# Kernel tuning notes

Measured on AMD Instinct MI355X. Metric: run time of the kernel, lower is better.

The kernel has to match this reference:

```python
import jax, jax.numpy as jnp
import numpy as np

E = 512        # embed_dim
H = 16         # num_heads
R = 8          # num_relation_heads
NH = H - R     # num_normal_heads
HD = E // H    # head_dim
SCALING = HD ** -0.5
B, LQ, LK = 2, 2048, 2048


def setup_inputs() -> dict:
    key = jax.random.key(0)
    ks = jax.random.split(key, 14)
    s = 1.0 / np.sqrt(E)  # keep pre-softmax logits moderate so exp() is stable
    inp = {
        "query": jax.random.normal(ks[0], (B, LQ, E), jnp.float32),
        "key": jax.random.normal(ks[1], (B, LK, E), jnp.float32),
        "value": jax.random.normal(ks[2], (B, LK, E), jnp.float32),
        "relation_weights": jax.random.uniform(ks[3], (B, R, LQ, LK), jnp.float32),
        "Wq": jax.random.normal(ks[4], (E, E), jnp.float32) * s,
        "bq": jnp.zeros((E,), jnp.float32),
        "Wk": jax.random.normal(ks[5], (E, E), jnp.float32) * s,
        "bk": jnp.zeros((E,), jnp.float32),
        "Wv": jax.random.normal(ks[6], (E, E), jnp.float32) * s,
        "bv": jnp.zeros((E,), jnp.float32),
        "Wo": jax.random.normal(ks[7], (E, E), jnp.float32) * s,
        "bo": jnp.zeros((E,), jnp.float32),
        "ln_gamma": jnp.ones((E,), jnp.float32),
        "ln_beta": jnp.zeros((E,), jnp.float32),
    }
    return inp


def reference(query, key, value, relation_weights, Wq, bq, Wk, bk, Wv, bv, Wo, bo, ln_gamma, ln_beta):
    b, lq, _ = query.shape
    lk = key.shape[1]
    # projections; weights stored as [in, out] so y = x @ W + b
    q = (query @ Wq + bq).reshape(b, lq, H, HD)
    k = (key @ Wk + bk).reshape(b, lk, H, HD)
    v = (value @ Wv + bv).reshape(b, lk, H, HD)
    # scores: [B, H, Lq, Lk]
    scores = jnp.einsum("bqhd,bkhd->bhqk", q, k) * SCALING
    # normal heads: standard softmax
    normal_attn = jax.nn.softmax(scores[:, :NH], axis=-1)
    # relation heads: exp(scores) * relation_weights, renormalized
    rel = jnp.exp(scores[:, NH:]) * relation_weights
    rel = rel / (rel.sum(axis=-1, keepdims=True) + 1e-6)
    attn = jnp.concatenate([normal_attn, rel], axis=1)  # [B, H, Lq, Lk]
    # weighted values -> [B, Lq, E]
    out = jnp.einsum("bhqk,bkhd->bqhd", attn, v).reshape(b, lq, E)
    out = out @ Wo + bo
    # LayerNorm (eps=1e-5, torch default)
    mu = out.mean(axis=-1, keepdims=True)
    var = out.var(axis=-1, keepdims=True)
    out = (out - mu) * jax.lax.rsqrt(var + 1e-5) * ln_gamma + ln_beta
    return out
```

## Files before the change

kernel.cpp:

```cpp
#include <hip/hip_runtime.h>


using u16 = unsigned short;
using u32 = unsigned int;

typedef __attribute__((ext_vector_type(8))) short bf16x8;
typedef __attribute__((ext_vector_type(4))) float f32x4;

#define H_  16
#define NH_ 8
#define HD_ 32
#define L_  2048
#define E_  512
#define B_  2
#define M_  4096
#define KSPLIT 2
static constexpr float SCALE_ = 0.1767766952966369f;

__device__ inline u16 f2bf(float x) {
  union { float f; u32 u; } v; v.f = x;
  u32 r = v.u + 0x7FFFu + ((v.u >> 16) & 1u);
  return (u16)(r >> 16);
}
__device__ inline float bf2f(u16 x) {
  union { u32 u; float f; } v; v.u = ((u32)x) << 16; return v.f;
}
__device__ inline u16 f2h(float x) {
  union { _Float16 h; u16 u; } v; v.h = (_Float16)x; return v.u;
}
__device__ inline float h2f(u16 x) {
  union { u16 u; _Float16 h; } v; v.u = x; return (float)v.h;
}

__global__ __launch_bounds__(256) void k_cvt3(const float* __restrict__ a, const float* __restrict__ b,
                                              const float* __restrict__ c,
                                              u16* __restrict__ oa, u16* __restrict__ ob, u16* __restrict__ oc) {
  int w = blockIdx.y;
  const float* s = (w == 0) ? a : (w == 1) ? b : c;
  u16* d = (w == 0) ? oa : (w == 1) ? ob : oc;
  size_t i = ((size_t)blockIdx.x * 256 + threadIdx.x) * 4;
  float4 v = *(const float4*)(s + i);
  uint2 pk;
  pk.x = (u32)f2bf(v.x) | ((u32)f2bf(v.y) << 16);
  pk.y = (u32)f2bf(v.z) | ((u32)f2bf(v.w) << 16);
  *(uint2*)(d + i) = pk;
}

__global__ __launch_bounds__(256) void k_wtrans(const float* __restrict__ Wq, const float* __restrict__ Wk,
                                                const float* __restrict__ Wv, const float* __restrict__ Wo,
                                                u16* __restrict__ Tq, u16* __restrict__ Tk,
                                                u16* __restrict__ Tv, u16* __restrict__ To) {
  int z = blockIdx.z;
  const float* W = (z == 0) ? Wq : (z == 1) ? Wk : (z == 2) ? Wv : Wo;
  u16* T = (z == 0) ? Tq : (z == 1) ? Tk : (z == 2) ? Tv : To;
  __shared__ u16 tile[64][65];
  int r0 = blockIdx.y * 64, c0 = blockIdx.x * 64;
  int tw = threadIdx.x >> 6, tl = threadIdx.x & 63;
#pragma unroll
  for (int i = 0; i < 16; ++i) {
    int r = i * 4 + tw;
    tile[r][tl] = f2bf(W[(size_t)(r0 + r) * E_ + c0 + tl]);
  }
  __syncthreads();
#pragma unroll
  for (int i = 0; i < 16; ++i) {
    int r = i * 4 + tw;
    T[(size_t)(c0 + r) * E_ + r0 + tl] = tile[tl][r];
  }
}

template <int MODE>
__device__ inline void gemm_body(const u16* __restrict__ A, const u16* __restrict__ Bt,
                                 const float* __restrict__ bias, void* __restrict__ out) {
  __shared__ __align__(16) u16 smem[2 * 128 * 72];
  u16* As = smem;
  u16* Bs = smem + 128 * 72;
  const int tid = threadIdx.x;
  const int lane = tid & 63, wid = tid >> 6;
  const int m0 = blockIdx.x * 128, n0 = blockIdx.y * 128;
  const int wm = (wid >> 1) * 64, wn = (wid & 1) * 64;
  const int mrow = lane & 15, quad = lane >> 4;
  f32x4 acc[4][4] = {};
  for (int k0 = 0; k0 < 512; k0 += 64) {
    __syncthreads();
#pragma unroll
    for (int i = 0; i < 4; ++i) {
      int task = i * 256 + tid;
      int r = task >> 3, c = task & 7;
      *(uint4*)(As + r * 72 + c * 8) = *(const uint4*)(A + (size_t)(m0 + r) * 512 + k0 + c * 8);
      *(uint4*)(Bs + r * 72 + c * 8) = *(const uint4*)(Bt + (size_t)(n0 + r) * 512 + k0 + c * 8);
    }
    __syncthreads();
#pragma unroll
    for (int kk = 0; kk < 64; kk += 32) {
      bf16x8 af[4], bfr[4];
#pragma unroll
      for (int f = 0; f < 4; ++f)
        af[f] = *(const bf16x8*)(As + (wm + f * 16 + mrow) * 72 + kk + quad * 8);
#pragma unroll
      for (int f = 0; f < 4; ++f)
        bfr[f] = *(const bf16x8*)(Bs + (wn + f * 16 + mrow) * 72 + kk + quad * 8);
#pragma unroll
      for (int fm = 0; fm < 4; ++fm)
#pragma unroll
        for (int fn = 0; fn < 4; ++fn)
          acc[fm][fn] = __builtin_amdgcn_mfma_f32_16x16x32_bf16(af[fm], bfr[fn], acc[fm][fn], 0, 0, 0);
    }
  }
  if (MODE == 0) {
    __syncthreads();
    u16* wscr = smem + wid * (64 * 72);
#pragma unroll
    for (int fn = 0; fn < 4; ++fn) {
      float bv = bias[n0 + wn + fn * 16 + mrow];
#pragma unroll
      for (int fm = 0; fm < 4; ++fm)
#pragma unroll
        for (int r = 0; r < 4; ++r)
          wscr[(fm * 16 + quad * 4 + r) * 72 + fn * 16 + mrow] = f2bf(acc[fm][fn][r] + bv);
    }
    asm volatile("s_waitcnt lgkmcnt(0)" ::: "memory");
    const int hg0 = (n0 + wn) >> 5;
#pragma unroll
    for (int c = 0; c < 8; ++c) {
      int linear = c * 64 + lane;
      int hh = linear >> 8;
      int rem = linear & 255;
      int lm = rem >> 2, j = rem & 3;
      uint4 vv = *(const uint4*)(wscr + lm * 72 + hh * 32 + j * 8);
      int gm = m0 + wm + lm;
      int bb = gm >> 11, q = gm & (L_ - 1);
      *(uint4*)((u16*)out + (((size_t)(bb * H_ + hg0 + hh)) * L_ + q) * HD_ + j * 8) = vv;
    }
  } else {
#pragma unroll
    for (int fn = 0; fn < 4; ++fn) {
      int gn = n0 + wn + fn * 16 + mrow;
      float bv = bias[gn];
#pragma unroll
      for (int fm = 0; fm < 4; ++fm)
#pragma unroll
        for (int r = 0; r < 4; ++r) {
          int gm = m0 + wm + fm * 16 + quad * 4 + r;
          ((float*)out)[(size_t)gm * E_ + gn] = acc[fm][fn][r] + bv;
        }
    }
  }
}

__global__ __launch_bounds__(256) void k_gemm_qkv(const u16* Xq, const u16* Xk, const u16* Xv,
                                                  const u16* Tq, const u16* Tk, const u16* Tv,
                                                  const float* bq, const float* bk, const float* bv,
                                                  u16* Qb, u16* Kb, u16* Vb) {
  int z = blockIdx.z;
  const u16* A = (z == 0) ? Xq : (z == 1) ? Xk : Xv;
  const u16* T = (z == 0) ? Tq : (z == 1) ? Tk : Tv;
  const float* bi = (z == 0) ? bq : (z == 1) ? bk : bv;
  u16* o = (z == 0) ? Qb : (z == 1) ? Kb : Vb;
  gemm_body<0>(A, T, bi, o);
}

__global__ __launch_bounds__(256) void k_gemm_o(const u16* A, const u16* T, const float* bi, float* Y) {
  gemm_body<1>(A, T, bi, Y);
}

__global__ __launch_bounds__(256) void k_attn(const u16* __restrict__ Qb, const u16* __restrict__ Kb,
                                              const u16* __restrict__ Vb, const float* __restrict__ relw,
                                              u16* __restrict__ Pnum, float* __restrict__ Pden) {
  const int tid = threadIdx.x, lane = tid & 63, wid = tid >> 6;
  const int q0 = blockIdx.x * 64;
  const int h = blockIdx.y;
  const int b = blockIdx.z & (B_ - 1), s = blockIdx.z >> 1;
  const int kbase = s * (L_ / KSPLIT);
  const bool isrel = (h >= NH_);
  const size_t headOff = ((size_t)(b * H_ + h)) * L_ * HD_;
  const float* wbase = isrel ? relw + ((size_t)(b * (H_ - NH_) + (h - NH_))) * L_ * L_ : nullptr;

  __shared__ __align__(16) u16 Qs[64 * 40];
  __shared__ __align__(16) u16 Ks[64 * 40];
  __shared__ __align__(16) u16 Vts[32 * 72];
  __shared__ __align__(16) u16 Ps[4][16 * 72];
  __shared__ __align__(16) u16 Ws[64 * 68];

  {
    int r = tid >> 2, c = tid & 3;
    *(uint4*)(Qs + r * 40 + c * 8) = *(const uint4*)(Qb + headOff + (size_t)(q0 + r) * HD_ + c * 8);
  }
  __syncthreads();
  const int mrow = lane & 15, quad = lane >> 4;
  bf16x8 qa = *(const bf16x8*)(Qs + (wid * 16 + mrow) * 40 + quad * 8);
  f32x4 accd[2] = {};
  float den[4] = {0.f, 0.f, 0.f, 0.f};

  for (int kt = kbase; kt < kbase + L_ / KSPLIT; kt += 64) {
    __syncthreads();
    if (tid < 128) {
      int p = tid >> 2, c = tid & 3;
      const u16* vsrc = Vb + headOff + (size_t)(kt + 2 * p) * HD_ + c * 8;
      uint4 v0 = *(const uint4*)(vsrc);
      uint4 v1 = *(const uint4*)(vsrc + HD_);
      const u16* s0 = (const u16*)&v0;
      const u16* s1 = (const u16*)&v1;
#pragma unroll
      for (int i = 0; i < 8; ++i) {
        u32 pk = (u32)s0[i] | ((u32)s1[i] << 16);
        *(u32*)(Vts + (c * 8 + i) * 72 + 2 * p) = pk;
      }
    } else {
      int t2 = tid - 128;
#pragma unroll
      for (int i = 0; i < 2; ++i) {
        int task = t2 * 2 + i;
        int r = task >> 2, c = task & 3;
        *(uint4*)(Ks + r * 40 + c * 8) = *(const uint4*)(Kb + headOff + (size_t)(kt + r) * HD_ + c * 8);
      }
    }
    if (isrel) {
      int q = tid >> 2, kc = (tid & 3) * 4;
      const float* wsrc = wbase + (size_t)(q0 + q) * L_ + kt + kc;
#pragma unroll
      for (int j = 0; j < 4; ++j) {
        float4 w4 = *(const float4*)(wsrc + j * 16);
        uint2 pk;
        pk.x = (u32)f2bf(w4.x) | ((u32)f2bf(w4.y) << 16);
        pk.y = (u32)f2bf(w4.z) | ((u32)f2bf(w4.w) << 16);
        *(uint2*)(Ws + q * 68 + kc + j * 16) = pk;
      }
    }
    __syncthreads();

    u16* pw = Ps[wid];
#pragma unroll
    for (int f = 0; f < 4; ++f) {
      bf16x8 kb = *(const bf16x8*)(Ks + (f * 16 + mrow) * 40 + quad * 8);
      f32x4 z = {0.f, 0.f, 0.f, 0.f};
      f32x4 sc = __builtin_amdgcn_mfma_f32_16x16x32_bf16(qa, kb, z, 0, 0, 0);
#pragma unroll
      for (int r = 0; r < 4; ++r) {
        float e = __expf(sc[r] * SCALE_);
        if (isrel)
          e *= bf2f(Ws[(wid * 16 + quad * 4 + r) * 68 + f * 16 + mrow]);
        den[r] += e;
        pw[(quad * 4 + r) * 72 + f * 16 + mrow] = f2bf(e);
      }
    }
    asm volatile("s_waitcnt lgkmcnt(0)" ::: "memory");
#pragma unroll
    for (int kk = 0; kk < 2; ++kk) {
      bf16x8 pa = *(const bf16x8*)(pw + mrow * 72 + kk * 32 + quad * 8);
#pragma unroll
      for (int dh = 0; dh < 2; ++dh) {
        bf16x8 vbf = *(const bf16x8*)(Vts + (dh * 16 + mrow) * 72 + kk * 32 + quad * 8);
        accd[dh] = __builtin_amdgcn_mfma_f32_16x16x32_bf16(pa, vbf, accd[dh], 0, 0, 0);
      }
    }
  }

#pragma unroll
  for (int off = 1; off < 16; off <<= 1)
#pragma unroll
    for (int r = 0; r < 4; ++r) den[r] += __shfl_xor(den[r], off, 64);

  const size_t pidx = ((size_t)(s * B_ + b) * H_ + h) * L_;
#pragma unroll
  for (int dh = 0; dh < 2; ++dh)
#pragma unroll
    for (int r = 0; r < 4; ++r) {
      int qg = q0 + wid * 16 + quad * 4 + r;
      Pnum[(pidx + qg) * HD_ + dh * 16 + mrow] = f2h(accd[dh][r]);
    }
  if (mrow == 0) {
    int qg = q0 + wid * 16 + quad * 4;
    float4 dv = {den[0], den[1], den[2], den[3]};
    *(float4*)(Pden + pidx + qg) = dv;
  }
}

__global__ __launch_bounds__(256) void k_combine(const u16* __restrict__ Pnum, const float* __restrict__ Pden,
                                                 u16* __restrict__ AO) {
  int row = blockIdx.x;
  int tid = threadIdx.x;
  int b = row >> 11, q = row & (L_ - 1);
  int e0 = tid * 2;
  int h = e0 >> 5, d = e0 & (HD_ - 1);
  size_t i0 = ((size_t)(0 * B_ + b) * H_ + h) * L_ + q;
  size_t i1 = ((size_t)(1 * B_ + b) * H_ + h) * L_ + q;
  u32 n0 = *(const u32*)(Pnum + i0 * HD_ + d);
  u32 n1 = *(const u32*)(Pnum + i1 * HD_ + d);
  float den = Pden[i0] + Pden[i1] + ((h >= NH_) ? 1e-6f : 0.f);
  float rinv = 1.0f / den;
  float x = (h2f((u16)n0) + h2f((u16)n1)) * rinv;
  float y = (h2f((u16)(n0 >> 16)) + h2f((u16)(n1 >> 16))) * rinv;
  u32 pk = (u32)f2bf(x) | ((u32)f2bf(y) << 16);
  *(u32*)(AO + (size_t)row * E_ + e0) = pk;
}

__global__ __launch_bounds__(256) void k_ln(const float* __restrict__ Y, const float* __restrict__ gamma,
                                            const float* __restrict__ beta, float* __restrict__ out) {
  int row = blockIdx.x, tid = threadIdx.x;
  const float* y = Y + (size_t)row * E_;
  float2 v = *(const float2*)(y + tid * 2);
  float s = v.x + v.y, sq = v.x * v.x + v.y * v.y;
#pragma unroll
  for (int off = 1; off < 64; off <<= 1) {
    s += __shfl_xor(s, off, 64);
    sq += __shfl_xor(sq, off, 64);
  }
  __shared__ float ss[4], ssq[4];
  int wid = tid >> 6, lane = tid & 63;
  if (lane == 0) { ss[wid] = s; ssq[wid] = sq; }
  __syncthreads();
  s = ss[0] + ss[1] + ss[2] + ss[3];
  sq = ssq[0] + ssq[1] + ssq[2] + ssq[3];
  float mean = s * (1.f / E_);
  float var = sq * (1.f / E_) - mean * mean;
  float rstd = rsqrtf(var + 1e-5f);
  float2 g = *(const float2*)(gamma + tid * 2);
  float2 be = *(const float2*)(beta + tid * 2);
  float2 o;
  o.x = (v.x - mean) * rstd * g.x + be.x;
  o.y = (v.y - mean) * rstd * g.y + be.y;
  *(float2*)(out + (size_t)row * E_ + tid * 2) = o;
}

extern "C" void kernel_launch(void* const* d_in, const int* in_sizes, int n_in,
                              void* d_out, int out_size, void* d_ws, size_t ws_size,
                              hipStream_t stream) {
  const float* query = (const float*)d_in[0];
  const float* key   = (const float*)d_in[1];
  const float* value = (const float*)d_in[2];
  const float* relw  = (const float*)d_in[3];
  const float* Wq = (const float*)d_in[4];
  const float* bq = (const float*)d_in[5];
  const float* Wk = (const float*)d_in[6];
  const float* bk = (const float*)d_in[7];
  const float* Wv = (const float*)d_in[8];
  const float* bv = (const float*)d_in[9];
  const float* Wo = (const float*)d_in[10];
  const float* bo = (const float*)d_in[11];
  const float* gamma = (const float*)d_in[12];
  const float* beta  = (const float*)d_in[13];

  char* ws = (char*)d_ws;
  u16* Xq = (u16*)(ws + 0);
  u16* Xk = (u16*)(ws + 4194304);
  u16* Xv = (u16*)(ws + 8388608);
  u16* Tq = (u16*)(ws + 12582912);
  u16* Tk = (u16*)(ws + 13107200);
  u16* Tv = (u16*)(ws + 13631488);
  u16* To = (u16*)(ws + 14155776);
  u16* Qb = (u16*)(ws + 14680064);
  u16* Kb = (u16*)(ws + 18874368);
  u16* Vb = (u16*)(ws + 23068672);
  u16* AO = (u16*)(ws + 27262976);
  u16*   Pnum = (u16*)(ws + 0);
  float* Pden = (float*)(ws + 8388608);
  float* Y = (float*)(ws + 0);

  k_cvt3<<<dim3(2048, 3, 1), 256, 0, stream>>>(query, key, value, Xq, Xk, Xv);
  k_wtrans<<<dim3(8, 8, 4), 256, 0, stream>>>(Wq, Wk, Wv, Wo, Tq, Tk, Tv, To);
  k_gemm_qkv<<<dim3(32, 4, 3), 256, 0, stream>>>(Xq, Xk, Xv, Tq, Tk, Tv, bq, bk, bv, Qb, Kb, Vb);
  k_attn<<<dim3(32, 16, B_ * KSPLIT), 256, 0, stream>>>(Qb, Kb, Vb, relw, Pnum, Pden);
  k_combine<<<M_, 256, 0, stream>>>(Pnum, Pden, AO);
  k_gemm_o<<<dim3(32, 4, 1), 256, 0, stream>>>(AO, To, bo, Y);
  k_ln<<<M_, 256, 0, stream>>>(Y, gamma, beta, (float*)d_out);
}
```

Measured before the change: 494.0 us.

## Prefetch next K/V/relation tiles into registers and shrink attention LDS footprint

The attention kernel now issues global loads for the next key tile's K, V and relation weights into registers right after the barrier, so they overlap with the current tile's MFMA and exp work. It also aliases the Q staging buffer with the relation-weight buffer, tightens LDS row strides, and sets a launch-bounds occupancy hint of 6 so more blocks can share a CU. The cost is extra live registers (two uint4 plus four float4) and possible LDS bank conflicts from the new padding strides.

```diff
diff --git a/kernel.cpp b/kernel.cpp
--- a/kernel.cpp
+++ b/kernel.cpp
@@ -164,75 +164,96 @@
   gemm_body<1>(A, T, bi, Y);
 }
 
-__global__ __launch_bounds__(256) void k_attn(const u16* __restrict__ Qb, const u16* __restrict__ Kb,
-                                              const u16* __restrict__ Vb, const float* __restrict__ relw,
-                                              u16* __restrict__ Pnum, float* __restrict__ Pden) {
+__global__ __launch_bounds__(256, 6) void k_attn(const u16* __restrict__ Qb, const u16* __restrict__ Kb,
+                                                 const u16* __restrict__ Vb, const float* __restrict__ relw,
+                                                 u16* __restrict__ Pnum, float* __restrict__ Pden) {
   const int tid = threadIdx.x, lane = tid & 63, wid = tid >> 6;
   const int q0 = blockIdx.x * 64;
   const int h = blockIdx.y;
   const int b = blockIdx.z & (B_ - 1), s = blockIdx.z >> 1;
   const int kbase = s * (L_ / KSPLIT);
+  const int kend = kbase + L_ / KSPLIT;
   const bool isrel = (h >= NH_);
   const size_t headOff = ((size_t)(b * H_ + h)) * L_ * HD_;
   const float* wbase = isrel ? relw + ((size_t)(b * (H_ - NH_) + (h - NH_))) * L_ * L_ : nullptr;
 
-  __shared__ __align__(16) u16 Qs[64 * 40];
-  __shared__ __align__(16) u16 Ks[64 * 40];
-  __shared__ __align__(16) u16 Vts[32 * 72];
-  __shared__ __align__(16) u16 Ps[4][16 * 72];
-  __shared__ __align__(16) u16 Ws[64 * 68];
+  __shared__ __align__(16) u16 QW[64 * 68];
+  __shared__ __align__(16) u16 Ks[64 * 36];
+  __shared__ __align__(16) u16 Vts[32 * 68];
+  __shared__ __align__(16) u16 Ps[4 * 16 * 68];
 
   {
     int r = tid >> 2, c = tid & 3;
-    *(uint4*)(Qs + r * 40 + c * 8) = *(const uint4*)(Qb + headOff + (size_t)(q0 + r) * HD_ + c * 8);
+    *(uint4*)(QW + r * 40 + c * 8) = *(const uint4*)(Qb + headOff + (size_t)(q0 + r) * HD_ + c * 8);
   }
   __syncthreads();
   const int mrow = lane & 15, quad = lane >> 4;
-  bf16x8 qa = *(const bf16x8*)(Qs + (wid * 16 + mrow) * 40 + quad * 8);
+  bf16x8 qa = *(const bf16x8*)(QW + (wid * 16 + mrow) * 40 + quad * 8);
   f32x4 accd[2] = {};
   float den[4] = {0.f, 0.f, 0.f, 0.f};
 
-  for (int kt = kbase; kt < kbase + L_ / KSPLIT; kt += 64) {
+  const int vp = tid >> 2, vc = tid & 3;
+  const int t2 = tid - 128;
+  const int kr = t2 >> 1, kc0 = (t2 & 1) * 2;
+  const int wq = tid >> 2, wkc = (tid & 3) * 4;
+  u16* Ws = QW;
+  u16* pw = Ps + wid * (16 * 68);
+
+  uint4 kv0, kv1;
+  float4 wreg0, wreg1, wreg2, wreg3;
+
+#define LOAD_REGS(KT)                                                                   \
+  do {                                                                                  \
+    if (tid < 128) {                                                                    \
+      const u16* vsrc = Vb + headOff + (size_t)((KT) + 2 * vp) * HD_ + vc * 8;          \
+      kv0 = *(const uint4*)(vsrc);                                                      \
+      kv1 = *(const uint4*)(vsrc + HD_);                                                \
+    } else {                                                                            \
+      const u16* ksrc = Kb + headOff + (size_t)((KT) + kr) * HD_ + kc0 * 8;             \
+      kv0 = *(const uint4*)(ksrc);                                                      \
+      kv1 = *(const uint4*)(ksrc + 8);                                                  \
+    }                                                                                   \
+    if (isrel) {                                                                        \
+      const float* wsrc = wbase + (size_t)(q0 + wq) * L_ + (KT) + wkc;                  \
+      wreg0 = *(const float4*)(wsrc);                                                   \
+      wreg1 = *(const float4*)(wsrc + 16);                                              \
+      wreg2 = *(const float4*)(wsrc + 32);                                              \
+      wreg3 = *(const float4*)(wsrc + 48);                                              \
+    }                                                                                   \
+  } while (0)
+
+  LOAD_REGS(kbase);
+
+  for (int kt = kbase; kt < kend; kt += 64) {
     __syncthreads();
     if (tid < 128) {
-      int p = tid >> 2, c = tid & 3;
-      const u16* vsrc = Vb + headOff + (size_t)(kt + 2 * p) * HD_ + c * 8;
-      uint4 v0 = *(const uint4*)(vsrc);
-      uint4 v1 = *(const uint4*)(vsrc + HD_);
-      const u16* s0 = (const u16*)&v0;
-      const u16* s1 = (const u16*)&v1;
+      const u16* s0 = (const u16*)&kv0;
+      const u16* s1 = (const u16*)&kv1;
 #pragma unroll
       for (int i = 0; i < 8; ++i) {
         u32 pk = (u32)s0[i] | ((u32)s1[i] << 16);
-        *(u32*)(Vts + (c * 8 + i) * 72 + 2 * p) = pk;
+        *(u32*)(Vts + (vc * 8 + i) * 68 + 2 * vp) = pk;
       }
     } else {
-      int t2 = tid - 128;
-#pragma unroll
-      for (int i = 0; i < 2; ++i) {
-        int task = t2 * 2 + i;
-        int r = task >> 2, c = task & 3;
-        *(uint4*)(Ks + r * 40 + c * 8) = *(const uint4*)(Kb + headOff + (size_t)(kt + r) * HD_ + c * 8);
+      *(uint4*)(Ks + kr * 36 + kc0 * 8) = kv0;
+      *(uint4*)(Ks + kr * 36 + kc0 * 8 + 8) = kv1;
+    }
+    if (isrel) {
+      const float4 wr[4] = {wreg0, wreg1, wreg2, wreg3};
+#pragma unroll
+      for (int j = 0; j < 4; ++j) {
+        uint2 pk;
+        pk.x = (u32)f2bf(wr[j].x) | ((u32)f2bf(wr[j].y) << 16);
+        pk.y = (u32)f2bf(wr[j].z) | ((u32)f2bf(wr[j].w) << 16);
+        *(uint2*)(Ws + wq * 68 + wkc + j * 16) = pk;
       }
     }
-    if (isrel) {
-      int q = tid >> 2, kc = (tid & 3) * 4;
-      const float* wsrc = wbase + (size_t)(q0 + q) * L_ + kt + kc;
-#pragma unroll
-      for (int j = 0; j < 4; ++j) {
-        float4 w4 = *(const float4*)(wsrc + j * 16);
-        uint2 pk;
-        pk.x = (u32)f2bf(w4.x) | ((u32)f2bf(w4.y) << 16);
-        pk.y = (u32)f2bf(w4.z) | ((u32)f2bf(w4.w) << 16);
-        *(uint2*)(Ws + q * 68 + kc + j * 16) = pk;
-      }
-    }
-    __syncthreads();
-
-    u16* pw = Ps[wid];
+    __syncthreads();
+    if (kt + 64 < kend) LOAD_REGS(kt + 64);
+
 #pragma unroll
     for (int f = 0; f < 4; ++f) {
-      bf16x8 kb = *(const bf16x8*)(Ks + (f * 16 + mrow) * 40 + quad * 8);
+      bf16x8 kb = *(const bf16x8*)(Ks + (f * 16 + mrow) * 36 + quad * 8);
       f32x4 z = {0.f, 0.f, 0.f, 0.f};
       f32x4 sc = __builtin_amdgcn_mfma_f32_16x16x32_bf16(qa, kb, z, 0, 0, 0);
 #pragma unroll
@@ -241,20 +262,21 @@
         if (isrel)
           e *= bf2f(Ws[(wid * 16 + quad * 4 + r) * 68 + f * 16 + mrow]);
         den[r] += e;
-        pw[(quad * 4 + r) * 72 + f * 16 + mrow] = f2bf(e);
+        pw[(quad * 4 + r) * 68 + f * 16 + mrow] = f2bf(e);
       }
     }
     asm volatile("s_waitcnt lgkmcnt(0)" ::: "memory");
 #pragma unroll
     for (int kk = 0; kk < 2; ++kk) {
-      bf16x8 pa = *(const bf16x8*)(pw + mrow * 72 + kk * 32 + quad * 8);
+      bf16x8 pa = *(const bf16x8*)(pw + mrow * 68 + kk * 32 + quad * 8);
 #pragma unroll
       for (int dh = 0; dh < 2; ++dh) {
-        bf16x8 vbf = *(const bf16x8*)(Vts + (dh * 16 + mrow) * 72 + kk * 32 + quad * 8);
+        bf16x8 vbf = *(const bf16x8*)(Vts + (dh * 16 + mrow) * 68 + kk * 32 + quad * 8);
         accd[dh] = __builtin_amdgcn_mfma_f32_16x16x32_bf16(pa, vbf, accd[dh], 0, 0, 0);
       }
     }
   }
+#undef LOAD_REGS
 
 #pragma unroll
   for (int off = 1; off < 16; off <<= 1)
```

Result: slower. 541.3 us (+9.6%).

## Pre-transpose V and load K/V/weights directly into registers in attention

Applied to the files above, without the earlier changes.

Adds a separate kernel that transposes V into a [head, d, L] layout. The attention kernel then loads K, V and the relation weights straight from global memory into per-wave registers instead of staging them in shared memory behind block-wide barriers. This removes both __syncthreads per key tile and the in-kernel V transpose, so each wave runs independently. In exchange it adds a kernel launch and extra V traffic, uses more registers, and reads relation weights uncoalesced as scalar fp32 loads (now kept in fp32 rather than rounded to bf16).

```diff
diff --git a/kernel.cpp b/kernel.cpp
--- a/kernel.cpp
+++ b/kernel.cpp
@@ -21,9 +21,6 @@
   union { float f; u32 u; } v; v.f = x;
   u32 r = v.u + 0x7FFFu + ((v.u >> 16) & 1u);
   return (u16)(r >> 16);
-}
-__device__ inline float bf2f(u16 x) {
-  union { u32 u; float f; } v; v.u = ((u32)x) << 16; return v.f;
 }
 __device__ inline u16 f2h(float x) {
   union { _Float16 h; u16 u; } v; v.h = (_Float16)x; return v.u;
@@ -164,95 +161,90 @@
   gemm_body<1>(A, T, bi, Y);
 }
 
+__global__ __launch_bounds__(256) void k_vtrans(const u16* __restrict__ Vb, u16* __restrict__ Vt) {
+  __shared__ u16 t[32 * 72];
+  const int q0 = blockIdx.x * 64;
+  const size_t headOff = (size_t)blockIdx.y * (L_ * HD_);
+  const int tid = threadIdx.x;
+  {
+    int q = tid >> 2, c = tid & 3;
+    uint4 v = *(const uint4*)(Vb + headOff + (size_t)(q0 + q) * HD_ + c * 8);
+    const u16* s = (const u16*)&v;
+#pragma unroll
+    for (int i = 0; i < 8; ++i) t[(c * 8 + i) * 72 + q] = s[i];
+  }
+  __syncthreads();
+  {
+    int d = tid >> 3, j = tid & 7;
+    uint4 o = *(const uint4*)(t + d * 72 + j * 8);
+    *(uint4*)(Vt + headOff + (size_t)d * L_ + q0 + j * 8) = o;
+  }
+}
+
 __global__ __launch_bounds__(256) void k_attn(const u16* __restrict__ Qb, const u16* __restrict__ Kb,
-                                              const u16* __restrict__ Vb, const float* __restrict__ relw,
+                                              const u16* __restrict__ Vt, const float* __restrict__ relw,
                                               u16* __restrict__ Pnum, float* __restrict__ Pden) {
   const int tid = threadIdx.x, lane = tid & 63, wid = tid >> 6;
   const int q0 = blockIdx.x * 64;
   const int h = blockIdx.y;
   const int b = blockIdx.z & (B_ - 1), s = blockIdx.z >> 1;
   const int kbase = s * (L_ / KSPLIT);
+  const int kend = kbase + L_ / KSPLIT;
   const bool isrel = (h >= NH_);
   const size_t headOff = ((size_t)(b * H_ + h)) * L_ * HD_;
   const float* wbase = isrel ? relw + ((size_t)(b * (H_ - NH_) + (h - NH_))) * L_ * L_ : nullptr;
 
-  __shared__ __align__(16) u16 Qs[64 * 40];
-  __shared__ __align__(16) u16 Ks[64 * 40];
-  __shared__ __align__(16) u16 Vts[32 * 72];
-  __shared__ __align__(16) u16 Ps[4][16 * 72];
-  __shared__ __align__(16) u16 Ws[64 * 68];
-
-  {
-    int r = tid >> 2, c = tid & 3;
-    *(uint4*)(Qs + r * 40 + c * 8) = *(const uint4*)(Qb + headOff + (size_t)(q0 + r) * HD_ + c * 8);
-  }
-  __syncthreads();
+  __shared__ __align__(16) u16 Ps[4 * 16 * 68];
+  u16* pw = Ps + wid * (16 * 68);
+
   const int mrow = lane & 15, quad = lane >> 4;
-  bf16x8 qa = *(const bf16x8*)(Qs + (wid * 16 + mrow) * 40 + quad * 8);
+  const int qrow = q0 + wid * 16;
+  bf16x8 qa = *(const bf16x8*)(Qb + headOff + (size_t)(qrow + mrow) * HD_ + quad * 8);
   f32x4 accd[2] = {};
   float den[4] = {0.f, 0.f, 0.f, 0.f};
 
-  for (int kt = kbase; kt < kbase + L_ / KSPLIT; kt += 64) {
-    __syncthreads();
-    if (tid < 128) {
-      int p = tid >> 2, c = tid & 3;
-      const u16* vsrc = Vb + headOff + (size_t)(kt + 2 * p) * HD_ + c * 8;
-      uint4 v0 = *(const uint4*)(vsrc);
-      uint4 v1 = *(const uint4*)(vsrc + HD_);
-      const u16* s0 = (const u16*)&v0;
-      const u16* s1 = (const u16*)&v1;
-#pragma unroll
-      for (int i = 0; i < 8; ++i) {
-        u32 pk = (u32)s0[i] | ((u32)s1[i] << 16);
-        *(u32*)(Vts + (c * 8 + i) * 72 + 2 * p) = pk;
+  for (int kt = kbase; kt < kend; kt += 64) {
+    bf16x8 kb[4];
+#pragma unroll
+    for (int f = 0; f < 4; ++f)
+      kb[f] = *(const bf16x8*)(Kb + headOff + (size_t)(kt + f * 16 + mrow) * HD_ + quad * 8);
+    bf16x8 vbf[2][2];
+#pragma unroll
+    for (int kk = 0; kk < 2; ++kk)
+#pragma unroll
+      for (int dh = 0; dh < 2; ++dh)
+        vbf[kk][dh] = *(const bf16x8*)(Vt + headOff + (size_t)(dh * 16 + mrow) * L_ + kt + kk * 32 + quad * 8);
+    float wv[4][4];
+    if (isrel) {
+#pragma unroll
+      for (int f = 0; f < 4; ++f)
+#pragma unroll
+        for (int r = 0; r < 4; ++r)
+          wv[f][r] = wbase[(size_t)(qrow + quad * 4 + r) * L_ + kt + f * 16 + mrow];
+    }
+
+    f32x4 sc[4];
+#pragma unroll
+    for (int f = 0; f < 4; ++f) {
+      f32x4 z = {0.f, 0.f, 0.f, 0.f};
+      sc[f] = __builtin_amdgcn_mfma_f32_16x16x32_bf16(qa, kb[f], z, 0, 0, 0);
+    }
+#pragma unroll
+    for (int f = 0; f < 4; ++f)
+#pragma unroll
+      for (int r = 0; r < 4; ++r) {
+        float e = __expf(sc[f][r] * SCALE_);
+        if (isrel) e *= wv[f][r];
+        den[r] += e;
+        pw[(quad * 4 + r) * 68 + f * 16 + mrow] = f2bf(e);
       }
-    } else {
-      int t2 = tid - 128;
-#pragma unroll
-      for (int i = 0; i < 2; ++i) {
-        int task = t2 * 2 + i;
-        int r = task >> 2, c = task & 3;
-        *(uint4*)(Ks + r * 40 + c * 8) = *(const uint4*)(Kb + headOff + (size_t)(kt + r) * HD_ + c * 8);
-      }
-    }
-    if (isrel) {
-      int q = tid >> 2, kc = (tid & 3) * 4;
-      const float* wsrc = wbase + (size_t)(q0 + q) * L_ + kt + kc;
-#pragma unroll
-      for (int j = 0; j < 4; ++j) {
-        float4 w4 = *(const float4*)(wsrc + j * 16);
-        uint2 pk;
-        pk.x = (u32)f2bf(w4.x) | ((u32)f2bf(w4.y) << 16);
-        pk.y = (u32)f2bf(w4.z) | ((u32)f2bf(w4.w) << 16);
-        *(uint2*)(Ws + q * 68 + kc + j * 16) = pk;
-      }
-    }
-    __syncthreads();
-
-    u16* pw = Ps[wid];
-#pragma unroll
-    for (int f = 0; f < 4; ++f) {
-      bf16x8 kb = *(const bf16x8*)(Ks + (f * 16 + mrow) * 40 + quad * 8);
-      f32x4 z = {0.f, 0.f, 0.f, 0.f};
-      f32x4 sc = __builtin_amdgcn_mfma_f32_16x16x32_bf16(qa, kb, z, 0, 0, 0);
-#pragma unroll
-      for (int r = 0; r < 4; ++r) {
-        float e = __expf(sc[r] * SCALE_);
-        if (isrel)
-          e *= bf2f(Ws[(wid * 16 + quad * 4 + r) * 68 + f * 16 + mrow]);
-        den[r] += e;
-        pw[(quad * 4 + r) * 72 + f * 16 + mrow] = f2bf(e);
-      }
-    }
     asm volatile("s_waitcnt lgkmcnt(0)" ::: "memory");
 #pragma unroll
     for (int kk = 0; kk < 2; ++kk) {
-      bf16x8 pa = *(const bf16x8*)(pw + mrow * 72 + kk * 32 + quad * 8);
-#pragma unroll
-      for (int dh = 0; dh < 2; ++dh) {
-        bf16x8 vbf = *(const bf16x8*)(Vts + (dh * 16 + mrow) * 72 + kk * 32 + quad * 8);
-        accd[dh] = __builtin_amdgcn_mfma_f32_16x16x32_bf16(pa, vbf, accd[dh], 0, 0, 0);
-      }
+      bf16x8 pa = *(const bf16x8*)(pw + mrow * 68 + kk * 32 + quad * 8);
+#pragma unroll
+      for (int dh = 0; dh < 2; ++dh)
+        accd[dh] = __builtin_amdgcn_mfma_f32_16x16x32_bf16(pa, vbf[kk][dh], accd[dh], 0, 0, 0);
     }
   }
 
@@ -266,11 +258,11 @@
   for (int dh = 0; dh < 2; ++dh)
 #pragma unroll
     for (int r = 0; r < 4; ++r) {
-      int qg = q0 + wid * 16 + quad * 4 + r;
+      int qg = qrow + quad * 4 + r;
       Pnum[(pidx + qg) * HD_ + dh * 16 + mrow] = f2h(accd[dh][r]);
     }
   if (mrow == 0) {
-    int qg = q0 + wid * 16 + quad * 4;
+    int qg = qrow + quad * 4;
     float4 dv = {den[0], den[1], den[2], den[3]};
     *(float4*)(Pden + pidx + qg) = dv;
   }
@@ -353,6 +345,7 @@
   u16* Kb = (u16*)(ws + 18874368);
   u16* Vb = (u16*)(ws + 23068672);
   u16* AO = (u16*)(ws + 27262976);
+  u16* Vt = (u16*)(ws + 31457280);
   u16*   Pnum = (u16*)(ws + 0);
   float* Pden = (float*)(ws + 8388608);
   float* Y = (float*)(ws + 0);
@@ -360,7 +353,8 @@
   k_cvt3<<<dim3(2048, 3, 1), 256, 0, stream>>>(query, key, value, Xq, Xk, Xv);
   k_wtrans<<<dim3(8, 8, 4), 256, 0, stream>>>(Wq, Wk, Wv, Wo, Tq, Tk, Tv, To);
   k_gemm_qkv<<<dim3(32, 4, 3), 256, 0, stream>>>(Xq, Xk, Xv, Tq, Tk, Tv, bq, bk, bv, Qb, Kb, Vb);
-  k_attn<<<dim3(32, 16, B_ * KSPLIT), 256, 0, stream>>>(Qb, Kb, Vb, relw, Pnum, Pden);
+  k_vtrans<<<dim3(32, 32, 1), 256, 0, stream>>>(Vb, Vt);
+  k_attn<<<dim3(32, 16, B_ * KSPLIT), 256, 0, stream>>>(Qb, Kb, Vt, relw, Pnum, Pden);
   k_combine<<<M_, 256, 0, stream>>>(Pnum, Pden, AO);
   k_gemm_o<<<dim3(32, 4, 1), 256, 0, stream>>>(AO, To, bo, Y);
   k_ln<<<M_, 256, 0, stream>>>(Y, gamma, beta, (float*)d_out);
```

After: 513.5 us. +3.9%, slower.
